# Kernel optimization log

Hardware: AMD Instinct MI355X
Metric: run time of the kernel (lower is better)

## Reference

```python
import jax, jax.numpy as jnp
import numpy as np

EMB_DIM = 4096
OUT_DIM = 4096
T_PREV = 8192


def setup_inputs() -> dict:
    key = jax.random.key(0)
    ks = jax.random.split(key, 6)
    return {
        "x": jax.random.normal(ks[0], (1, EMB_DIM), dtype=jnp.float32),
        "W_query": jax.random.normal(ks[1], (OUT_DIM, EMB_DIM), dtype=jnp.float32) * 0.02,
        "W_key": jax.random.normal(ks[2], (OUT_DIM, EMB_DIM), dtype=jnp.float32) * 0.02,
        "W_value": jax.random.normal(ks[3], (OUT_DIM, EMB_DIM), dtype=jnp.float32) * 0.02,
        "K_cache": jax.random.normal(ks[4], (OUT_DIM, T_PREV), dtype=jnp.float32),
        "V_cache": jax.random.normal(ks[5], (OUT_DIM, T_PREV), dtype=jnp.float32),
    }


def reference(x, W_query, W_key, W_value, K_cache, V_cache):
    # x: [1, E] -> xt: [E, 1]
    xt = x.T
    q = W_query @ xt  # [D, 1]
    k = W_key @ xt    # [D, 1]
    v = W_value @ xt  # [D, 1]
    # append current step to caches (hstack semantics)
    K = jnp.concatenate([K_cache, k], axis=1)  # [D, T+1]
    V = jnp.concatenate([V_cache, v], axis=1)  # [D, T+1]
    # sigmoid-scored attention (NOT softmax)
    a = (q.reshape(1, -1) @ K) / jnp.sqrt(jnp.float32(OUT_DIM))  # [1, T+1]
    a = jax.nn.sigmoid(a)
    z = V @ a.reshape(-1, 1)  # [D, 1]
    return z
```

## Files before the change

### kernel.cpp

```cpp
#include <hip/hip_runtime.h>
#include <math.h>

#define EMB   4096
#define DIM   4096
#define TPREV 8192
#define TTOT  8193

#define WS_Q        0
#define WS_K        DIM
#define WS_V        (2*DIM)
#define WS_A        (3*DIM)
#define WS_PART     20544
#define NCHUNK      128
#define CHUNK_ROWS  32

__device__ __forceinline__ float dot4(float4 a, float4 b) {
    return a.x * b.x + a.y * b.y + a.z * b.z + a.w * b.w;
}

__global__ __launch_bounds__(256) void qkv_kernel(
    const float* __restrict__ x,
    const float* __restrict__ Wq, const float* __restrict__ Wk,
    const float* __restrict__ Wv, float* __restrict__ ws) {
    int b = blockIdx.x;
    int m = b >> 12;
    int r = b & 4095;
    const float* W = (m == 0) ? Wq : (m == 1) ? Wk : Wv;
    const float4* row = (const float4*)(W + (size_t)r * EMB);
    const float4* xv  = (const float4*)x;
    int tid = threadIdx.x;

    float4 w0 = row[tid];
    float4 w1 = row[tid + 256];
    float4 w2 = row[tid + 512];
    float4 w3 = row[tid + 768];
    float4 x0 = xv[tid];
    float4 x1 = xv[tid + 256];
    float4 x2 = xv[tid + 512];
    float4 x3 = xv[tid + 768];

    float s = dot4(w0, x0) + dot4(w1, x1) + dot4(w2, x2) + dot4(w3, x3);

#pragma unroll
    for (int off = 32; off > 0; off >>= 1) s += __shfl_down(s, off, 64);

    __shared__ float red[4];
    if ((tid & 63) == 0) red[tid >> 6] = s;
    __syncthreads();
    if (tid == 0) ws[m * DIM + r] = red[0] + red[1] + red[2] + red[3];
}

__global__ __launch_bounds__(256) void score_kernel(
    const float* __restrict__ Kc, float* __restrict__ ws) {
    const float* q = ws + WS_Q;
    float* part    = ws + WS_PART;

    __shared__ float qs[CHUNK_ROWS];
    int d0 = blockIdx.y * CHUNK_ROWS;
    if (threadIdx.x < CHUNK_ROWS) qs[threadIdx.x] = q[d0 + threadIdx.x];
    __syncthreads();

    size_t t = (size_t)blockIdx.x * 1024 + threadIdx.x * 4;
    const float* base = Kc + (size_t)d0 * TPREV + t;

    float4 acc = {0.f, 0.f, 0.f, 0.f};
#pragma unroll
    for (int g = 0; g < CHUNK_ROWS / 4; ++g) {
        float4 k0 = *(const float4*)(base + (size_t)(4 * g + 0) * TPREV);
        float4 k1 = *(const float4*)(base + (size_t)(4 * g + 1) * TPREV);
        float4 k2 = *(const float4*)(base + (size_t)(4 * g + 2) * TPREV);
        float4 k3 = *(const float4*)(base + (size_t)(4 * g + 3) * TPREV);
        float q0 = qs[4 * g], q1 = qs[4 * g + 1], q2 = qs[4 * g + 2], q3 = qs[4 * g + 3];
        acc.x += q0 * k0.x + q1 * k1.x + q2 * k2.x + q3 * k3.x;
        acc.y += q0 * k0.y + q1 * k1.y + q2 * k2.y + q3 * k3.y;
        acc.z += q0 * k0.z + q1 * k1.z + q2 * k2.z + q3 * k3.z;
        acc.w += q0 * k0.w + q1 * k1.w + q2 * k2.w + q3 * k3.w;
    }
    *(float4*)(part + (size_t)blockIdx.y * TPREV + t) = acc;
}

__global__ __launch_bounds__(256) void reduce_sigmoid_kernel(
    float* __restrict__ ws) {
    if (blockIdx.x < 64) {
        const float4* p = (const float4*)(ws + WS_PART);
        int f4    = threadIdx.x & 31;
        int slice = threadIdx.x >> 5;
        size_t idx = (size_t)(slice * 16) * (TPREV / 4) + (size_t)blockIdx.x * 32 + f4;

        float4 s = {0.f, 0.f, 0.f, 0.f};
#pragma unroll 4
        for (int c = 0; c < 16; ++c) {
            float4 v = p[idx + (size_t)c * (TPREV / 4)];
            s.x += v.x; s.y += v.y; s.z += v.z; s.w += v.w;
        }
        __shared__ float4 red[256];
        red[threadIdx.x] = s;
        __syncthreads();
        if (threadIdx.x < 32) {
            float4 tot = red[threadIdx.x];
#pragma unroll
            for (int sl = 1; sl < 8; ++sl) {
                float4 v = red[sl * 32 + threadIdx.x];
                tot.x += v.x; tot.y += v.y; tot.z += v.z; tot.w += v.w;
            }
            tot.x = 1.0f / (1.0f + __expf(-tot.x * 0.015625f));
            tot.y = 1.0f / (1.0f + __expf(-tot.y * 0.015625f));
            tot.z = 1.0f / (1.0f + __expf(-tot.z * 0.015625f));
            tot.w = 1.0f / (1.0f + __expf(-tot.w * 0.015625f));
            ((float4*)(ws + WS_A))[(size_t)blockIdx.x * 32 + threadIdx.x] = tot;
        }
    } else {
        const float* q = ws + WS_Q;
        const float* k = ws + WS_K;
        float s = 0.0f;
        int base = threadIdx.x * 16;
#pragma unroll 16
        for (int i = 0; i < 16; ++i) s += q[base + i] * k[base + i];
        __shared__ float red[256];
        red[threadIdx.x] = s;
        __syncthreads();
        for (int off = 128; off > 0; off >>= 1) {
            if (threadIdx.x < off) red[threadIdx.x] += red[threadIdx.x + off];
            __syncthreads();
        }
        if (threadIdx.x == 0) {
            float v = red[0] * 0.015625f;
            ws[WS_A + TPREV] = 1.0f / (1.0f + __expf(-v));
        }
    }
}

__global__ __launch_bounds__(256) void out_kernel(
    const float* __restrict__ Vc, const float* __restrict__ ws,
    float* __restrict__ out) {
    int d = blockIdx.x;
    const float4* row = (const float4*)(Vc + (size_t)d * TPREV);
    const float4* av  = (const float4*)(ws + WS_A);
    int tid = threadIdx.x;

    float s = 0.0f;
#pragma unroll
    for (int g = 0; g < 2; ++g) {
        int o = g * 1024;
        float4 v0 = row[o + tid];
        float4 v1 = row[o + tid + 256];
        float4 v2 = row[o + tid + 512];
        float4 v3 = row[o + tid + 768];
        float4 a0 = av[o + tid];
        float4 a1 = av[o + tid + 256];
        float4 a2 = av[o + tid + 512];
        float4 a3 = av[o + tid + 768];
        s += dot4(v0, a0) + dot4(v1, a1) + dot4(v2, a2) + dot4(v3, a3);
    }

#pragma unroll
    for (int off = 32; off > 0; off >>= 1) s += __shfl_down(s, off, 64);

    __shared__ float red[4];
    if ((tid & 63) == 0) red[tid >> 6] = s;
    __syncthreads();
    if (tid == 0)
        out[d] = red[0] + red[1] + red[2] + red[3]
               + ws[WS_V + d] * ws[WS_A + TPREV];
}

extern "C" void kernel_launch(void* const* d_in, const int* in_sizes, int n_in,
                              void* d_out, int out_size, void* d_ws, size_t ws_size,
                              hipStream_t stream) {
    const float* x  = (const float*)d_in[0];
    const float* Wq = (const float*)d_in[1];
    const float* Wk = (const float*)d_in[2];
    const float* Wv = (const float*)d_in[3];
    const float* Kc = (const float*)d_in[4];
    const float* Vc = (const float*)d_in[5];
    float* out = (float*)d_out;
    float* ws  = (float*)d_ws;

    qkv_kernel<<<12288, 256, 0, stream>>>(x, Wq, Wk, Wv, ws);
    score_kernel<<<dim3(8, 128), 256, 0, stream>>>(Kc, ws);
    reduce_sigmoid_kernel<<<65, 256, 0, stream>>>(ws);
    out_kernel<<<4096, 256, 0, stream>>>(Vc, ws, out);
}
```

Measured before the change: 389.9 us.

## Fuse all stages into one cooperative kernel with grid syncs

Replaces the four separate launches with a single cooperative persistent kernel of 1024 blocks that runs the QKV projection, the score partials, the reduce/sigmoid and the output matvec, separated by grid-wide syncs. x is staged in shared memory and each wave handles one row for the matvecs. This removes inter-kernel launch gaps and tail effects, at the cost of grid-sync overhead and a fixed occupancy that may limit memory-level parallelism. The old multi-kernel path is kept as a fallback if the cooperative launch fails.

```diff
diff --git a/kernel.cpp b/kernel.cpp
--- a/kernel.cpp
+++ b/kernel.cpp
@@ -1,21 +1,164 @@
 #include <hip/hip_runtime.h>
+#include <hip/hip_cooperative_groups.h>
 #include <math.h>
+
+namespace cg = cooperative_groups;
 
 #define EMB   4096
 #define DIM   4096
 #define TPREV 8192
-#define TTOT  8193
-
-#define WS_Q        0
-#define WS_K        DIM
-#define WS_V        (2*DIM)
-#define WS_A        (3*DIM)
-#define WS_PART     20544
+
+#define WS_Q    0
+#define WS_K    DIM
+#define WS_V    (2*DIM)
+#define WS_A    (3*DIM)
+#define WS_PART 20544
 #define NCHUNK      128
 #define CHUNK_ROWS  32
 
 __device__ __forceinline__ float dot4(float4 a, float4 b) {
     return a.x * b.x + a.y * b.y + a.z * b.z + a.w * b.w;
+}
+
+__global__ __launch_bounds__(256, 4) void fused_kernel(
+    const float* __restrict__ x,
+    const float* __restrict__ Wq, const float* __restrict__ Wk,
+    const float* __restrict__ Wv,
+    const float* __restrict__ Kc, const float* __restrict__ Vc,
+    float* __restrict__ ws, float* __restrict__ out) {
+
+    cg::grid_group grid = cg::this_grid();
+    __shared__ __align__(16) float smem[4096];
+    float4* sm4 = (float4*)smem;
+
+    const int tid  = threadIdx.x;
+    const int lane = tid & 63;
+    const int wave = tid >> 6;
+    const int b    = blockIdx.x;
+
+    {
+        const float4* xg = (const float4*)x;
+        sm4[tid]       = xg[tid];
+        sm4[tid + 256] = xg[tid + 256];
+        sm4[tid + 512] = xg[tid + 512];
+        sm4[tid + 768] = xg[tid + 768];
+        __syncthreads();
+
+        int gw = b * 4 + wave;
+        const float* Ws[3]  = {Wq, Wk, Wv};
+        const int    off[3] = {WS_Q, WS_K, WS_V};
+#pragma unroll
+        for (int m = 0; m < 3; ++m) {
+            const float4* row = (const float4*)(Ws[m] + (size_t)gw * EMB);
+            float s = 0.f;
+#pragma unroll
+            for (int g = 0; g < 4; ++g) {
+                int base = g * 256 + lane;
+                float4 w0 = row[base];
+                float4 w1 = row[base + 64];
+                float4 w2 = row[base + 128];
+                float4 w3 = row[base + 192];
+                s += dot4(w0, sm4[base])       + dot4(w1, sm4[base + 64])
+                   + dot4(w2, sm4[base + 128]) + dot4(w3, sm4[base + 192]);
+            }
+#pragma unroll
+            for (int o = 32; o > 0; o >>= 1) s += __shfl_down(s, o, 64);
+            if (lane == 0) ws[off[m] + gw] = s;
+        }
+    }
+    grid.sync();
+
+    {
+        int tt    = b >> 7;
+        int chunk = b & 127;
+        if (tid < CHUNK_ROWS) smem[tid] = ws[WS_Q + chunk * CHUNK_ROWS + tid];
+        __syncthreads();
+        size_t t4 = (size_t)tt * 256 + tid;
+        const float4* kc4 = (const float4*)Kc;
+        float4 acc = {0.f, 0.f, 0.f, 0.f};
+#pragma unroll
+        for (int g = 0; g < CHUNK_ROWS / 4; ++g) {
+            int r0 = chunk * CHUNK_ROWS + g * 4;
+            float4 k0 = kc4[(size_t)(r0 + 0) * 2048 + t4];
+            float4 k1 = kc4[(size_t)(r0 + 1) * 2048 + t4];
+            float4 k2 = kc4[(size_t)(r0 + 2) * 2048 + t4];
+            float4 k3 = kc4[(size_t)(r0 + 3) * 2048 + t4];
+            float q0 = smem[g*4], q1 = smem[g*4+1], q2 = smem[g*4+2], q3 = smem[g*4+3];
+            acc.x += q0 * k0.x + q1 * k1.x + q2 * k2.x + q3 * k3.x;
+            acc.y += q0 * k0.y + q1 * k1.y + q2 * k2.y + q3 * k3.y;
+            acc.z += q0 * k0.z + q1 * k1.z + q2 * k2.z + q3 * k3.z;
+            acc.w += q0 * k0.w + q1 * k1.w + q2 * k2.w + q3 * k3.w;
+        }
+        ((float4*)(ws + WS_PART))[(size_t)chunk * 2048 + t4] = acc;
+    }
+    grid.sync();
+
+    if (b < 256) {
+        const float4* p4 = (const float4*)(ws + WS_PART);
+        int f4    = tid & 7;
+        int slice = tid >> 3;
+        size_t idx = (size_t)b * 8 + f4;
+        float4 s = {0.f, 0.f, 0.f, 0.f};
+#pragma unroll
+        for (int c = 0; c < 4; ++c) {
+            float4 v = p4[(size_t)(slice * 4 + c) * 2048 + idx];
+            s.x += v.x; s.y += v.y; s.z += v.z; s.w += v.w;
+        }
+        sm4[tid] = s;
+        __syncthreads();
+        if (tid < 8) {
+            float4 tot = {0.f, 0.f, 0.f, 0.f};
+#pragma unroll
+            for (int sl = 0; sl < 32; ++sl) {
+                float4 v = sm4[sl * 8 + tid];
+                tot.x += v.x; tot.y += v.y; tot.z += v.z; tot.w += v.w;
+            }
+            tot.x = 1.f / (1.f + __expf(-tot.x * 0.015625f));
+            tot.y = 1.f / (1.f + __expf(-tot.y * 0.015625f));
+            tot.z = 1.f / (1.f + __expf(-tot.z * 0.015625f));
+            tot.w = 1.f / (1.f + __expf(-tot.w * 0.015625f));
+            ((float4*)(ws + WS_A))[(size_t)b * 8 + tid] = tot;
+        }
+    } else if (b == 1023) {
+        const float* q = ws + WS_Q;
+        const float* k = ws + WS_K;
+        float s = 0.f;
+        int base = tid * 16;
+#pragma unroll
+        for (int i = 0; i < 16; ++i) s += q[base + i] * k[base + i];
+        smem[tid] = s;
+        __syncthreads();
+        for (int o = 128; o > 0; o >>= 1) {
+            if (tid < o) smem[tid] += smem[tid + o];
+            __syncthreads();
+        }
+        if (tid == 0) ws[WS_A + TPREV] = 1.f / (1.f + __expf(-smem[0] * 0.015625f));
+    }
+    grid.sync();
+
+    {
+        int r = b * 4 + wave;
+        const float4* vrow = (const float4*)(Vc + (size_t)r * TPREV);
+        const float4* a4   = (const float4*)(ws + WS_A);
+        float s = 0.f;
+#pragma unroll
+        for (int g = 0; g < 8; ++g) {
+            int base = g * 256 + lane;
+            float4 v0 = vrow[base];
+            float4 v1 = vrow[base + 64];
+            float4 v2 = vrow[base + 128];
+            float4 v3 = vrow[base + 192];
+            float4 a0 = a4[base];
+            float4 a1 = a4[base + 64];
+            float4 a2 = a4[base + 128];
+            float4 a3 = a4[base + 192];
+            s += dot4(v0, a0) + dot4(v1, a1) + dot4(v2, a2) + dot4(v3, a3);
+        }
+#pragma unroll
+        for (int o = 32; o > 0; o >>= 1) s += __shfl_down(s, o, 64);
+        if (lane == 0)
+            out[r] = s + ws[WS_V + r] * ws[WS_A + TPREV];
+    }
 }
 
 __global__ __launch_bounds__(256) void qkv_kernel(
@@ -40,10 +183,8 @@
     float4 x3 = xv[tid + 768];
 
     float s = dot4(w0, x0) + dot4(w1, x1) + dot4(w2, x2) + dot4(w3, x3);
-
 #pragma unroll
     for (int off = 32; off > 0; off >>= 1) s += __shfl_down(s, off, 64);
-
     __shared__ float red[4];
     if ((tid & 63) == 0) red[tid >> 6] = s;
     __syncthreads();
@@ -62,7 +203,6 @@
 
     size_t t = (size_t)blockIdx.x * 1024 + threadIdx.x * 4;
     const float* base = Kc + (size_t)d0 * TPREV + t;
-
     float4 acc = {0.f, 0.f, 0.f, 0.f};
 #pragma unroll
     for (int g = 0; g < CHUNK_ROWS / 4; ++g) {
@@ -86,7 +226,6 @@
         int f4    = threadIdx.x & 31;
         int slice = threadIdx.x >> 5;
         size_t idx = (size_t)(slice * 16) * (TPREV / 4) + (size_t)blockIdx.x * 32 + f4;
-
         float4 s = {0.f, 0.f, 0.f, 0.f};
 #pragma unroll 4
         for (int c = 0; c < 16; ++c) {
@@ -114,7 +253,7 @@
         const float* k = ws + WS_K;
         float s = 0.0f;
         int base = threadIdx.x * 16;
-#pragma unroll 16
+#pragma unroll
         for (int i = 0; i < 16; ++i) s += q[base + i] * k[base + i];
         __shared__ float red[256];
         red[threadIdx.x] = s;
@@ -137,7 +276,6 @@
     const float4* row = (const float4*)(Vc + (size_t)d * TPREV);
     const float4* av  = (const float4*)(ws + WS_A);
     int tid = threadIdx.x;
-
     float s = 0.0f;
 #pragma unroll
     for (int g = 0; g < 2; ++g) {
@@ -152,10 +290,8 @@
         float4 a3 = av[o + tid + 768];
         s += dot4(v0, a0) + dot4(v1, a1) + dot4(v2, a2) + dot4(v3, a3);
     }
-
 #pragma unroll
     for (int off = 32; off > 0; off >>= 1) s += __shfl_down(s, off, 64);
-
     __shared__ float red[4];
     if ((tid & 63) == 0) red[tid >> 6] = s;
     __syncthreads();
@@ -176,8 +312,14 @@
     float* out = (float*)d_out;
     float* ws  = (float*)d_ws;
 
-    qkv_kernel<<<12288, 256, 0, stream>>>(x, Wq, Wk, Wv, ws);
-    score_kernel<<<dim3(8, 128), 256, 0, stream>>>(Kc, ws);
-    reduce_sigmoid_kernel<<<65, 256, 0, stream>>>(ws);
-    out_kernel<<<4096, 256, 0, stream>>>(Vc, ws, out);
-}
+    void* args[] = {(void*)&x, (void*)&Wq, (void*)&Wk, (void*)&Wv,
+                    (void*)&Kc, (void*)&Vc, (void*)&ws, (void*)&out};
+    hipError_t err = hipLaunchCooperativeKernel((void*)fused_kernel, dim3(1024),
+                                                dim3(256), args, 0, stream);
+    if (err != hipSuccess) {
+        qkv_kernel<<<12288, 256, 0, stream>>>(x, Wq, Wk, Wv, ws);
+        score_kernel<<<dim3(8, 128), 256, 0, stream>>>(Kc, ws);
+        reduce_sigmoid_kernel<<<65, 256, 0, stream>>>(ws);
+        out_kernel<<<4096, 256, 0, stream>>>(Vc, ws, out);
+    }
+}
```

New measurement: 766.8 us. 1.97x slower.
